# Performance work log

Measured on AMD Instinct MI355X. Metric: run time of the kernel, lower is better.

## Reference

```python
import jax, jax.numpy as jnp
import numpy as np

EPS = 1e-14  # clamp floor from torch .clamp(1e-14)


def setup_inputs() -> dict:
    key = jax.random.key(0)
    kq, kk, kv, km = jax.random.split(key, 4)
    B, L, D = 16, 2048, 64
    q = jax.random.normal(kq, (B, L, D), dtype=jnp.float32)
    k = jax.random.normal(kk, (B, L, D), dtype=jnp.float32)
    v = jax.random.normal(kv, (B, L, D), dtype=jnp.float32)
    # boolean mask, True = masked-out position (score forced to 0 in 'dot' mode)
    attn_mask = jax.random.randint(km, (B, L, L), 0, 2).astype(jnp.bool_)
    return {"q": q, "k": k, "v": v, "attn_mask": attn_mask}


def reference(q, k, v, attn_mask):
    # kernel_type='dot': raw QK^T scores (no temperature scaling)
    attn = jnp.einsum('bqd,bkd->bqk', q, k)
    # masked positions set to 0 (not -inf) in the 'dot' path
    attn = jnp.where(attn_mask, jnp.zeros((), attn.dtype), attn)
    # sum-normalization instead of softmax: attn / attn.sum(-1).clamp(1e-14)
    denom = jnp.clip(jnp.sum(attn, axis=2, keepdims=True), EPS)
    attn = attn / denom
    # dropout is identity at inference (eval mode)
    output = jnp.einsum('bqk,bkd->bqd', attn, v)
    return output, attn
```

## Files before the change

kernel.cpp:

```cpp
#include <hip/hip_runtime.h>

#define Bb 16
#define Lq 2048
#define Dd 64
#define QT 32
#define NT 512

typedef _Float16 f16x2 __attribute__((ext_vector_type(2)));
typedef _Float16 f16x8 __attribute__((ext_vector_type(8)));
typedef __attribute__((ext_vector_type(4))) float f32x4;
typedef __attribute__((ext_vector_type(2))) float f32x2;
typedef __attribute__((ext_vector_type(4))) unsigned int u32x4;
typedef __attribute__((ext_vector_type(2))) unsigned int u32x2;
typedef __attribute__((ext_vector_type(4))) int i32x4;
typedef unsigned long long u64;
typedef __attribute__((ext_vector_type(2))) unsigned long long u64x2;

union H8 { f16x8 v8; f16x2 h2[4]; unsigned int u[4]; u32x4 u4; };
union H1 { f16x2 h; unsigned int u; };

__device__ __forceinline__ f16x2 pkrtz(float a, float b) {
  return __builtin_bit_cast(f16x2, __builtin_amdgcn_cvt_pkrtz(a, b));
}
__device__ __forceinline__ f32x4 MF16(f16x8 a, f16x8 b, f32x4 c) {
  return __builtin_amdgcn_mfma_f32_16x16x32_f16(a, b, c, 0, 0, 0);
}
__device__ __forceinline__ f32x4 MFu(u32x4 a, const H8& b, f32x4 c) {
  return MF16(__builtin_bit_cast(f16x8, a), b.v8, c);
}
__device__ __forceinline__ void gl_lds16(const void* g, void* l) {
  __builtin_amdgcn_global_load_lds(
      (const __attribute__((address_space(1))) void*)g,
      (__attribute__((address_space(3))) void*)l, 16, 0, 0);
}

__global__ __launch_bounds__(256)
void sdpa_prep(const float* __restrict__ kg, const float* __restrict__ vg,
               const i32x4* __restrict__ mg4,
               u32x4* __restrict__ Kw4, u32x4* __restrict__ Vq,
               u64* __restrict__ mb)
{
  const int t = threadIdx.x, blk = blockIdx.x;
  if (blk < 1024) {
    const int row = blk * 32 + (t >> 3);
    const int oct = t & 7;
    const int b = row >> 11, r = row & 2047;
    const int win = r >> 8, rw = r & 255;
    const float* kp = kg + (size_t)row * Dd + oct * 8;
    f32x4 a = *(const f32x4*)kp;
    f32x4 c = *(const f32x4*)(kp + 4);
    H1 h0, h1, h2, h3, l0, l1, l2, l3;
    h0.h = pkrtz(a.x, a.y); l0.h = pkrtz(a.x - (float)h0.h.x, a.y - (float)h0.h.y);
    h1.h = pkrtz(a.z, a.w); l1.h = pkrtz(a.z - (float)h1.h.x, a.w - (float)h1.h.y);
    h2.h = pkrtz(c.x, c.y); l2.h = pkrtz(c.x - (float)h2.h.x, c.y - (float)h2.h.y);
    h3.h = pkrtz(c.z, c.w); l3.h = pkrtz(c.z - (float)h3.h.x, c.w - (float)h3.h.y);
    u32x4 hh = {h0.u, h1.u, h2.u, h3.u};
    u32x4 ll = {l0.u, l1.u, l2.u, l3.u};
    const int sl = oct ^ (rw & 7);
    const size_t base = ((size_t)((b * 8 + win) * 256 + rw)) * 16;
    Kw4[base + sl] = hh;
    Kw4[base + 8 + sl] = ll;
  } else if (blk < 2048) {
    const int v_ = (blk - 1024) * 256 + t;
    const int ln = v_ & 15, nt = (v_ >> 4) & 3, u = (v_ >> 6) & 3;
    const int g = (v_ >> 8) & 7, w = (v_ >> 11) & 7, b = v_ >> 14;
    const int R = w * 256 + g * 32 + u * 4;
    const float* vp = vg + ((size_t)b * Lq + R) * Dd + nt * 16 + ln;
    H1 p0, p1, p2, p3;
    p0.h = pkrtz(vp[0 * Dd],  vp[1 * Dd]);
    p1.h = pkrtz(vp[2 * Dd],  vp[3 * Dd]);
    p2.h = pkrtz(vp[16 * Dd], vp[17 * Dd]);
    p3.h = pkrtz(vp[18 * Dd], vp[19 * Dd]);
    u32x4 o = {p0.u, p1.u, p2.u, p3.u};
    Vq[v_] = o;
  } else {
    const int l  = t & 63;
    const int wg = ((blk - 2048) << 2) | (t >> 6);
    i32x4 cur = __builtin_nontemporal_load(&mg4[((size_t)wg * 32) * 64 + l]);
#pragma unroll 1
    for (int it = 0; it < 32; ++it) {
      i32x4 nxt = {0, 0, 0, 0};
      if (it < 31) nxt = __builtin_nontemporal_load(&mg4[((size_t)wg * 32 + it + 1) * 64 + l]);
      u64 b0 = __ballot(cur.x != 0);
      u64 b1 = __ballot(cur.y != 0);
      u64 b2 = __ballot(cur.z != 0);
      u64 b3 = __ballot(cur.w != 0);
      if (l == 0) {
        u64* o = mb + ((size_t)wg * 32 + it) * 4;
        u64x2 w0 = {b0, b1}, w1 = {b2, b3};
        *(u64x2*)o = w0;
        *(u64x2*)(o + 2) = w1;
      }
      cur = nxt;
    }
  }
}

__global__ __launch_bounds__(NT, 2)
void sdpa_main(const float* __restrict__ qg, const char* __restrict__ Kw,
               const u32x4* __restrict__ Vqp, const u64* __restrict__ mbp,
               float* __restrict__ outO, float* __restrict__ outA)
{
  __shared__ char kbuf[2][65536];
  __shared__ unsigned int Qh[QT][36], Ql[QT][36];
  __shared__ float red[QT][4];
  __shared__ float dinv_s[QT];

  const int tid = threadIdx.x;
  const int l   = tid & 63;
  const int ln  = l & 15;
  const int u   = l >> 4;
  const int w   = tid >> 6;
  const int qt  = w >> 2;
  const int ks  = w & 3;
  const int bid = (int)(blockIdx.x % 8) * 128 + (int)(blockIdx.x / 8);
  const int b   = bid >> 6;
  const int q0  = (bid & 63) * QT;

  {
    int r = tid >> 4, i4 = tid & 15;
    f32x4 qv = *(const f32x4*)(qg + (size_t)(b * Lq + q0 + r) * Dd + 4 * i4);
    H1 ha, hb, la, lb;
    ha.h = pkrtz(qv.x, qv.y); la.h = pkrtz(qv.x - (float)ha.h.x, qv.y - (float)ha.h.y);
    hb.h = pkrtz(qv.z, qv.w); lb.h = pkrtz(qv.z - (float)hb.h.x, qv.w - (float)hb.h.y);
    Qh[r][2 * i4] = ha.u; Qh[r][2 * i4 + 1] = hb.u;
    Ql[r][2 * i4] = la.u; Ql[r][2 * i4 + 1] = lb.u;
  }

  const char* kwb = Kw + (size_t)b * 8 * 65536;
  auto STAGE = [&](int buf_, int win_) {
#pragma unroll
    for (int i = 0; i < 8; ++i)
      gl_lds16(kwb + (size_t)win_ * 65536 + i * 8192 + w * 1024 + l * 16,
               &kbuf[buf_][i * 8192 + w * 1024]);
  };
  STAGE(0, 0);
  __syncthreads();

  H8 Bh0, Bh1, Bl0, Bl1;
  Bh0.u4 = *(const u32x4*)&Qh[16 * qt + ln][4 * u];
  Bh1.u4 = *(const u32x4*)&Qh[16 * qt + ln][16 + 4 * u];
  Bl0.u4 = *(const u32x4*)&Ql[16 * qt + ln][4 * u];
  Bl1.u4 = *(const u32x4*)&Ql[16 * qt + ln][16 + 4 * u];

  const u64* mrow = mbp + (size_t)(b * Lq + q0 + 16 * qt + ln) * 32;
  unsigned int su[8][4][2];
  f32x4 pv[4] = {{0,0,0,0},{0,0,0,0},{0,0,0,0},{0,0,0,0}};
  float rs = 0.f;
  const int key  = ln & 7;
  const int rbase = ks * 64;
  const int shb  = u + ((ks & 1) << 4);
  const bool lowh = (ks < 2);

#pragma unroll
  for (int win = 0; win < 8; ++win) {
    const int cur = win & 1;
    if (win < 7) STAGE(cur ^ 1, win + 1);

    u32x4 vbuf[8];
    const u32x4* vq = Vqp + (size_t)(b * 8 + win) * 2048;
#pragma unroll
    for (int g2 = 0; g2 < 2; ++g2)
#pragma unroll
      for (int nt = 0; nt < 4; ++nt)
        vbuf[g2 * 4 + nt] = vq[(((ks * 2 + g2) * 4 + u) * 4 + nt) * 16 + ln];

    u32x4 MA = *(const u32x4*)(mrow + win * 4);
    u32x4 MC = *(const u32x4*)(mrow + win * 4 + 2);
    unsigned mw0 = lowh ? MA.x : MA.y;
    unsigned mw1 = lowh ? MA.z : MA.w;
    unsigned mw2 = lowh ? MC.x : MC.y;
    unsigned mw3 = lowh ? MC.z : MC.w;

    const char* kb_ = &kbuf[cur][0];
#pragma unroll
    for (int t = 0; t < 4; ++t) {
      const int rw = rbase + 16 * t + ln;
      const char* rp = kb_ + rw * 256;
      u32x4 h0  = *(const u32x4*)(rp + ((u ^ key) << 4));
      u32x4 h1  = *(const u32x4*)(rp + (((4 + u) ^ key) << 4));
      u32x4 l0_ = *(const u32x4*)(rp + ((8 | (u ^ key)) << 4));
      u32x4 l1_ = *(const u32x4*)(rp + ((8 | ((4 + u) ^ key)) << 4));
      f32x4 acc = {0.f, 0.f, 0.f, 0.f};
      acc = MFu(h0, Bh0, acc);
      acc = MFu(h0, Bl0, acc);
      acc = MFu(l0_, Bh0, acc);
      acc = MFu(h1, Bh1, acc);
      acc = MFu(h1, Bl1, acc);
      acc = MFu(l1_, Bh1, acc);
      const int sh = 4 * t + shb;
      float s0 = ((mw0 >> sh) & 1u) ? 0.f : acc.x;
      float s1 = ((mw1 >> sh) & 1u) ? 0.f : acc.y;
      float s2 = ((mw2 >> sh) & 1u) ? 0.f : acc.z;
      float s3 = ((mw3 >> sh) & 1u) ? 0.f : acc.w;
      rs += (s0 + s1) + (s2 + s3);
      H1 p0, p1;
      p0.h = pkrtz(s0, s1); p1.h = pkrtz(s2, s3);
      su[win][t][0] = p0.u; su[win][t][1] = p1.u;
    }
#pragma unroll
    for (int g2 = 0; g2 < 2; ++g2) {
      H8 aw;
      aw.u[0] = su[win][2 * g2][0];     aw.u[1] = su[win][2 * g2][1];
      aw.u[2] = su[win][2 * g2 + 1][0]; aw.u[3] = su[win][2 * g2 + 1][1];
      pv[0] = MF16(aw.v8, __builtin_bit_cast(f16x8, vbuf[g2 * 4 + 0]), pv[0]);
      pv[1] = MF16(aw.v8, __builtin_bit_cast(f16x8, vbuf[g2 * 4 + 1]), pv[1]);
      pv[2] = MF16(aw.v8, __builtin_bit_cast(f16x8, vbuf[g2 * 4 + 2]), pv[2]);
      pv[3] = MF16(aw.v8, __builtin_bit_cast(f16x8, vbuf[g2 * 4 + 3]), pv[3]);
    }
    __syncthreads();
  }

  rs += __shfl_xor(rs, 16);
  rs += __shfl_xor(rs, 32);
  if (l < 16) red[16 * qt + ln][ks] = rs;

  {
    char* Sb = &kbuf[0][0];
    const int row = 16 * qt + ln;
    char* srow = Sb + row * 4096;
    const unsigned skey = (unsigned)(row & 15) << 3;
#pragma unroll
    for (int win = 0; win < 8; ++win)
#pragma unroll
      for (int t = 0; t < 4; ++t) {
        unsigned Bo = 512u * win + 128u * ks + 32u * t + 8u * u;
        u32x2 pk2 = {su[win][t][0], su[win][t][1]};
        *(u32x2*)(srow + (Bo ^ skey)) = pk2;
      }
  }
  __syncthreads();
  if (tid < 32) {
    f32x4 r4 = *(const f32x4*)&red[tid][0];
    float s = (r4.x + r4.y) + (r4.z + r4.w);
    dinv_s[tid] = 1.0f / fmaxf(s, 1e-14f);
  }
  __syncthreads();

  {
    const char* Sb = &kbuf[0][0];
#pragma unroll
    for (int r = 0; r < 4; ++r) {
      const int rr = 4 * w + r;
      const float dv = dinv_s[rr];
      const char* sr = Sb + rr * 4096;
      const unsigned rk = (unsigned)(rr & 15) << 3;
      float* arow = outA + (size_t)(b * Lq + q0 + rr) * Lq;
#pragma unroll
      for (int m = 0; m < 8; ++m) {
        u32x2 pk = *(const u32x2*)(sr + ((unsigned)(512 * m + 8 * l) ^ rk));
        H1 a0, a1; a0.u = pk.x; a1.u = pk.y;
        f32x4 st = {(float)a0.h.x * dv, (float)a0.h.y * dv,
                    (float)a1.h.x * dv, (float)a1.h.y * dv};
        __builtin_nontemporal_store(st, (f32x4*)(arow + 256 * m + 4 * l));
      }
    }
  }
  __syncthreads();

  {
    float (*Or)[4][16][66] = (float (*)[4][16][66])&kbuf[0][0];
#pragma unroll
    for (int nt = 0; nt < 4; ++nt)
#pragma unroll
      for (int r2 = 0; r2 < 4; ++r2)
        Or[qt][ks][4 * u + r2][16 * nt + ln] = pv[nt][r2];
    __syncthreads();
#pragma unroll
    for (int i = 0; i < 2; ++i) {
      int item = tid + NT * i;
      int q_ = item >> 5, d = (item & 31) * 2;
      float o0 = 0.f, o1 = 0.f;
#pragma unroll
      for (int k2 = 0; k2 < 4; ++k2) {
        o0 += Or[q_ >> 4][k2][q_ & 15][d];
        o1 += Or[q_ >> 4][k2][q_ & 15][d + 1];
      }
      float dv = dinv_s[q_];
      f32x2 st = {o0 * dv, o1 * dv};
      *(f32x2*)(outO + (size_t)(b * Lq + q0 + q_) * Dd + d) = st;
    }
  }
}

extern "C" void kernel_launch(void* const* d_in, const int* in_sizes, int n_in,
                              void* d_out, int out_size, void* d_ws, size_t ws_size,
                              hipStream_t stream) {
  const float* q = (const float*)d_in[0];
  const float* k = (const float*)d_in[1];
  const float* v = (const float*)d_in[2];
  const int*   m = (const int*)d_in[3];
  float* outO = (float*)d_out;
  float* outA = outO + (size_t)Bb * Lq * Dd;

  char* ws = (char*)d_ws;
  u32x4* Kw4 = (u32x4*)ws;
  u32x4* Vq  = (u32x4*)(ws + (8u << 20));
  u64*   mb  = (u64*)(ws + (12u << 20));
  sdpa_prep<<<4096, 256, 0, stream>>>(k, v, (const i32x4*)m, Kw4, Vq, mb);
  sdpa_main<<<Bb * (Lq / QT), NT, 0, stream>>>(q, (const char*)Kw4, Vq, mb, outO, outA);
}
```

Before: 162.4 us.

## Defer PV MFMA to post-normalization pass and write attn directly from registers

Moves the P·V MFMA accumulation out of the QK score loop into a second loop that runs after the row sums are known. That second loop double-buffers V register loads one window ahead. The attention matrix is now written straight from the register-held fp16 scores, scaled by the inverse denominator, so the LDS staging round trip and its extra barriers go away. The cost is that each lane's stores now cover only 16-byte chunks within 64-float segments instead of fully contiguous 256-float row sweeps, which may hurt store coalescing. Register pressure also rises from the doubled V buffer.

```diff
diff --git a/kernel.cpp b/kernel.cpp
--- a/kernel.cpp
+++ b/kernel.cpp
@@ -145,25 +145,16 @@
 
   const u64* mrow = mbp + (size_t)(b * Lq + q0 + 16 * qt + ln) * 32;
   unsigned int su[8][4][2];
-  f32x4 pv[4] = {{0,0,0,0},{0,0,0,0},{0,0,0,0},{0,0,0,0}};
   float rs = 0.f;
-  const int key  = ln & 7;
+  const int key   = ln & 7;
   const int rbase = ks * 64;
-  const int shb  = u + ((ks & 1) << 4);
+  const int shb   = u + ((ks & 1) << 4);
   const bool lowh = (ks < 2);
 
 #pragma unroll
   for (int win = 0; win < 8; ++win) {
     const int cur = win & 1;
     if (win < 7) STAGE(cur ^ 1, win + 1);
-
-    u32x4 vbuf[8];
-    const u32x4* vq = Vqp + (size_t)(b * 8 + win) * 2048;
-#pragma unroll
-    for (int g2 = 0; g2 < 2; ++g2)
-#pragma unroll
-      for (int nt = 0; nt < 4; ++nt)
-        vbuf[g2 * 4 + nt] = vq[(((ks * 2 + g2) * 4 + u) * 4 + nt) * 16 + ln];
 
     u32x4 MA = *(const u32x4*)(mrow + win * 4);
     u32x4 MC = *(const u32x4*)(mrow + win * 4 + 2);
@@ -198,37 +189,12 @@
       p0.h = pkrtz(s0, s1); p1.h = pkrtz(s2, s3);
       su[win][t][0] = p0.u; su[win][t][1] = p1.u;
     }
-#pragma unroll
-    for (int g2 = 0; g2 < 2; ++g2) {
-      H8 aw;
-      aw.u[0] = su[win][2 * g2][0];     aw.u[1] = su[win][2 * g2][1];
-      aw.u[2] = su[win][2 * g2 + 1][0]; aw.u[3] = su[win][2 * g2 + 1][1];
-      pv[0] = MF16(aw.v8, __builtin_bit_cast(f16x8, vbuf[g2 * 4 + 0]), pv[0]);
-      pv[1] = MF16(aw.v8, __builtin_bit_cast(f16x8, vbuf[g2 * 4 + 1]), pv[1]);
-      pv[2] = MF16(aw.v8, __builtin_bit_cast(f16x8, vbuf[g2 * 4 + 2]), pv[2]);
-      pv[3] = MF16(aw.v8, __builtin_bit_cast(f16x8, vbuf[g2 * 4 + 3]), pv[3]);
-    }
     __syncthreads();
   }
 
   rs += __shfl_xor(rs, 16);
   rs += __shfl_xor(rs, 32);
   if (l < 16) red[16 * qt + ln][ks] = rs;
-
-  {
-    char* Sb = &kbuf[0][0];
-    const int row = 16 * qt + ln;
-    char* srow = Sb + row * 4096;
-    const unsigned skey = (unsigned)(row & 15) << 3;
-#pragma unroll
-    for (int win = 0; win < 8; ++win)
-#pragma unroll
-      for (int t = 0; t < 4; ++t) {
-        unsigned Bo = 512u * win + 128u * ks + 32u * t + 8u * u;
-        u32x2 pk2 = {su[win][t][0], su[win][t][1]};
-        *(u32x2*)(srow + (Bo ^ skey)) = pk2;
-      }
-  }
   __syncthreads();
   if (tid < 32) {
     f32x4 r4 = *(const f32x4*)&red[tid][0];
@@ -237,26 +203,47 @@
   }
   __syncthreads();
 
-  {
-    const char* Sb = &kbuf[0][0];
-#pragma unroll
-    for (int r = 0; r < 4; ++r) {
-      const int rr = 4 * w + r;
-      const float dv = dinv_s[rr];
-      const char* sr = Sb + rr * 4096;
-      const unsigned rk = (unsigned)(rr & 15) << 3;
-      float* arow = outA + (size_t)(b * Lq + q0 + rr) * Lq;
-#pragma unroll
-      for (int m = 0; m < 8; ++m) {
-        u32x2 pk = *(const u32x2*)(sr + ((unsigned)(512 * m + 8 * l) ^ rk));
-        H1 a0, a1; a0.u = pk.x; a1.u = pk.y;
-        f32x4 st = {(float)a0.h.x * dv, (float)a0.h.y * dv,
-                    (float)a1.h.x * dv, (float)a1.h.y * dv};
-        __builtin_nontemporal_store(st, (f32x4*)(arow + 256 * m + 4 * l));
-      }
-    }
-  }
-  __syncthreads();
+  f32x4 pv[4] = {{0,0,0,0},{0,0,0,0},{0,0,0,0},{0,0,0,0}};
+  const float dv = dinv_s[16 * qt + ln];
+  float* arow = outA + (size_t)(b * Lq + q0 + 16 * qt + ln) * Lq + ks * 64;
+
+  u32x4 vb[2][8];
+#pragma unroll
+  for (int g2 = 0; g2 < 2; ++g2)
+#pragma unroll
+    for (int nt = 0; nt < 4; ++nt)
+      vb[0][g2 * 4 + nt] =
+          Vqp[(size_t)(b * 8) * 2048 + (((ks * 2 + g2) * 4 + u) * 4 + nt) * 16 + ln];
+
+#pragma unroll
+  for (int win = 0; win < 8; ++win) {
+    const int c2 = win & 1;
+    if (win < 7) {
+      const u32x4* vqn = Vqp + (size_t)(b * 8 + win + 1) * 2048;
+#pragma unroll
+      for (int g2 = 0; g2 < 2; ++g2)
+#pragma unroll
+        for (int nt = 0; nt < 4; ++nt)
+          vb[c2 ^ 1][g2 * 4 + nt] = vqn[(((ks * 2 + g2) * 4 + u) * 4 + nt) * 16 + ln];
+    }
+#pragma unroll
+    for (int t = 0; t < 4; ++t) {
+      H1 p0, p1; p0.u = su[win][t][0]; p1.u = su[win][t][1];
+      f32x4 st = {(float)p0.h.x * dv, (float)p0.h.y * dv,
+                  (float)p1.h.x * dv, (float)p1.h.y * dv};
+      __builtin_nontemporal_store(st, (f32x4*)(arow + win * 256 + 16 * t + 4 * u));
+    }
+#pragma unroll
+    for (int g2 = 0; g2 < 2; ++g2) {
+      H8 aw;
+      aw.u[0] = su[win][2 * g2][0];     aw.u[1] = su[win][2 * g2][1];
+      aw.u[2] = su[win][2 * g2 + 1][0]; aw.u[3] = su[win][2 * g2 + 1][1];
+      pv[0] = MF16(aw.v8, __builtin_bit_cast(f16x8, vb[c2][g2 * 4 + 0]), pv[0]);
+      pv[1] = MF16(aw.v8, __builtin_bit_cast(f16x8, vb[c2][g2 * 4 + 1]), pv[1]);
+      pv[2] = MF16(aw.v8, __builtin_bit_cast(f16x8, vb[c2][g2 * 4 + 2]), pv[2]);
+      pv[3] = MF16(aw.v8, __builtin_bit_cast(f16x8, vb[c2][g2 * 4 + 3]), pv[3]);
+    }
+  }
 
   {
     float (*Or)[4][16][66] = (float (*)[4][16][66])&kbuf[0][0];
@@ -276,8 +263,8 @@
         o0 += Or[q_ >> 4][k2][q_ & 15][d];
         o1 += Or[q_ >> 4][k2][q_ & 15][d + 1];
       }
-      float dv = dinv_s[q_];
-      f32x2 st = {o0 * dv, o1 * dv};
+      float dvq = dinv_s[q_];
+      f32x2 st = {o0 * dvq, o1 * dvq};
       *(f32x2*)(outO + (size_t)(b * Lq + q0 + q_) * Dd + d) = st;
     }
   }
```

Measured after the change: 186.5 us. +14.9%, slower.

## Halve K window size to shrink LDS footprint and raise occupancy

Applied to the files above, without the earlier changes.

Splits the key dimension into 16 windows of 128 rows instead of 8 of 256, halving the double-buffered K LDS tile. The goal is to fit more workgroups per CU (launch bounds raised from 2 to 4 blocks). The attention-row writeback is restaged in two halves so the score buffer fits in the smaller LDS. The trade-offs are twice as many barriers and window iterations, a tighter register budget per thread, and extra syncs in the output phase.

```diff
diff --git a/kernel.cpp b/kernel.cpp
--- a/kernel.cpp
+++ b/kernel.cpp
@@ -5,6 +5,8 @@
 #define Dd 64
 #define QT 32
 #define NT 512
+#define NWIN 16
+#define WINB 32768
 
 typedef _Float16 f16x2 __attribute__((ext_vector_type(2)));
 typedef _Float16 f16x8 __attribute__((ext_vector_type(8)));
@@ -45,7 +47,7 @@
     const int row = blk * 32 + (t >> 3);
     const int oct = t & 7;
     const int b = row >> 11, r = row & 2047;
-    const int win = r >> 8, rw = r & 255;
+    const int win = r >> 7, rw = r & 127;
     const float* kp = kg + (size_t)row * Dd + oct * 8;
     f32x4 a = *(const f32x4*)kp;
     f32x4 c = *(const f32x4*)(kp + 4);
@@ -57,7 +59,7 @@
     u32x4 hh = {h0.u, h1.u, h2.u, h3.u};
     u32x4 ll = {l0.u, l1.u, l2.u, l3.u};
     const int sl = oct ^ (rw & 7);
-    const size_t base = ((size_t)((b * 8 + win) * 256 + rw)) * 16;
+    const size_t base = ((size_t)((b * 16 + win) * 128 + rw)) * 16;
     Kw4[base + sl] = hh;
     Kw4[base + 8 + sl] = ll;
   } else if (blk < 2048) {
@@ -96,12 +98,12 @@
   }
 }
 
-__global__ __launch_bounds__(NT, 2)
+__global__ __launch_bounds__(NT, 4)
 void sdpa_main(const float* __restrict__ qg, const char* __restrict__ Kw,
                const u32x4* __restrict__ Vqp, const u64* __restrict__ mbp,
                float* __restrict__ outO, float* __restrict__ outA)
 {
-  __shared__ char kbuf[2][65536];
+  __shared__ char kbuf[2][WINB];
   __shared__ unsigned int Qh[QT][36], Ql[QT][36];
   __shared__ float red[QT][4];
   __shared__ float dinv_s[QT];
@@ -127,11 +129,11 @@
     Ql[r][2 * i4] = la.u; Ql[r][2 * i4 + 1] = lb.u;
   }
 
-  const char* kwb = Kw + (size_t)b * 8 * 65536;
+  const char* kwb = Kw + (size_t)b * NWIN * WINB;
   auto STAGE = [&](int buf_, int win_) {
 #pragma unroll
-    for (int i = 0; i < 8; ++i)
-      gl_lds16(kwb + (size_t)win_ * 65536 + i * 8192 + w * 1024 + l * 16,
+    for (int i = 0; i < 4; ++i)
+      gl_lds16(kwb + (size_t)win_ * WINB + i * 8192 + w * 1024 + l * 16,
                &kbuf[buf_][i * 8192 + w * 1024]);
   };
   STAGE(0, 0);
@@ -144,37 +146,39 @@
   Bl1.u4 = *(const u32x4*)&Ql[16 * qt + ln][16 + 4 * u];
 
   const u64* mrow = mbp + (size_t)(b * Lq + q0 + 16 * qt + ln) * 32;
-  unsigned int su[8][4][2];
+  unsigned int su[NWIN][2][2];
   f32x4 pv[4] = {{0,0,0,0},{0,0,0,0},{0,0,0,0},{0,0,0,0}};
   float rs = 0.f;
-  const int key  = ln & 7;
-  const int rbase = ks * 64;
-  const int shb  = u + ((ks & 1) << 4);
-  const bool lowh = (ks < 2);
-
-#pragma unroll
-  for (int win = 0; win < 8; ++win) {
+  const int key   = ln & 7;
+  const int rbase = ks * 32;
+  u32x4 MA, MC;
+
+#pragma unroll
+  for (int win = 0; win < NWIN; ++win) {
     const int cur = win & 1;
-    if (win < 7) STAGE(cur ^ 1, win + 1);
-
-    u32x4 vbuf[8];
-    const u32x4* vq = Vqp + (size_t)(b * 8 + win) * 2048;
-#pragma unroll
-    for (int g2 = 0; g2 < 2; ++g2)
+    if (win < NWIN - 1) STAGE(cur ^ 1, win + 1);
+
+    if ((win & 1) == 0) {
+      MA = *(const u32x4*)(mrow + (win >> 1) * 4);
+      MC = *(const u32x4*)(mrow + (win >> 1) * 4 + 2);
+    }
+    unsigned mw0 = (win & 1) ? MA.y : MA.x;
+    unsigned mw1 = (win & 1) ? MA.w : MA.z;
+    unsigned mw2 = (win & 1) ? MC.y : MC.x;
+    unsigned mw3 = (win & 1) ? MC.w : MC.z;
+
+    u32x4 vbuf[4];
+    {
+      const u32x4* vq = Vqp + (size_t)(b * 8 + (win >> 1)) * 2048;
+      const int g_old = (win & 1) * 4 + ks;
 #pragma unroll
       for (int nt = 0; nt < 4; ++nt)
-        vbuf[g2 * 4 + nt] = vq[(((ks * 2 + g2) * 4 + u) * 4 + nt) * 16 + ln];
-
-    u32x4 MA = *(const u32x4*)(mrow + win * 4);
-    u32x4 MC = *(const u32x4*)(mrow + win * 4 + 2);
-    unsigned mw0 = lowh ? MA.x : MA.y;
-    unsigned mw1 = lowh ? MA.z : MA.w;
-    unsigned mw2 = lowh ? MC.x : MC.y;
-    unsigned mw3 = lowh ? MC.z : MC.w;
+        vbuf[nt] = vq[((g_old * 4 + u) * 4 + nt) * 16 + ln];
+    }
 
     const char* kb_ = &kbuf[cur][0];
 #pragma unroll
-    for (int t = 0; t < 4; ++t) {
+    for (int t = 0; t < 2; ++t) {
       const int rw = rbase + 16 * t + ln;
       const char* rp = kb_ + rw * 256;
       u32x4 h0  = *(const u32x4*)(rp + ((u ^ key) << 4));
@@ -188,7 +192,7 @@
       acc = MFu(h1, Bh1, acc);
       acc = MFu(h1, Bl1, acc);
       acc = MFu(l1_, Bh1, acc);
-      const int sh = 4 * t + shb;
+      const int sh = ks * 8 + 4 * t + u;
       float s0 = ((mw0 >> sh) & 1u) ? 0.f : acc.x;
       float s1 = ((mw1 >> sh) & 1u) ? 0.f : acc.y;
       float s2 = ((mw2 >> sh) & 1u) ? 0.f : acc.z;
@@ -198,15 +202,14 @@
       p0.h = pkrtz(s0, s1); p1.h = pkrtz(s2, s3);
       su[win][t][0] = p0.u; su[win][t][1] = p1.u;
     }
-#pragma unroll
-    for (int g2 = 0; g2 < 2; ++g2) {
+    {
       H8 aw;
-      aw.u[0] = su[win][2 * g2][0];     aw.u[1] = su[win][2 * g2][1];
-      aw.u[2] = su[win][2 * g2 + 1][0]; aw.u[3] = su[win][2 * g2 + 1][1];
-      pv[0] = MF16(aw.v8, __builtin_bit_cast(f16x8, vbuf[g2 * 4 + 0]), pv[0]);
-      pv[1] = MF16(aw.v8, __builtin_bit_cast(f16x8, vbuf[g2 * 4 + 1]), pv[1]);
-      pv[2] = MF16(aw.v8, __builtin_bit_cast(f16x8, vbuf[g2 * 4 + 2]), pv[2]);
-      pv[3] = MF16(aw.v8, __builtin_bit_cast(f16x8, vbuf[g2 * 4 + 3]), pv[3]);
+      aw.u[0] = su[win][0][0]; aw.u[1] = su[win][0][1];
+      aw.u[2] = su[win][1][0]; aw.u[3] = su[win][1][1];
+      pv[0] = MF16(aw.v8, __builtin_bit_cast(f16x8, vbuf[0]), pv[0]);
+      pv[1] = MF16(aw.v8, __builtin_bit_cast(f16x8, vbuf[1]), pv[1]);
+      pv[2] = MF16(aw.v8, __builtin_bit_cast(f16x8, vbuf[2]), pv[2]);
+      pv[3] = MF16(aw.v8, __builtin_bit_cast(f16x8, vbuf[3]), pv[3]);
     }
     __syncthreads();
   }
@@ -214,21 +217,6 @@
   rs += __shfl_xor(rs, 16);
   rs += __shfl_xor(rs, 32);
   if (l < 16) red[16 * qt + ln][ks] = rs;
-
-  {
-    char* Sb = &kbuf[0][0];
-    const int row = 16 * qt + ln;
-    char* srow = Sb + row * 4096;
-    const unsigned skey = (unsigned)(row & 15) << 3;
-#pragma unroll
-    for (int win = 0; win < 8; ++win)
-#pragma unroll
-      for (int t = 0; t < 4; ++t) {
-        unsigned Bo = 512u * win + 128u * ks + 32u * t + 8u * u;
-        u32x2 pk2 = {su[win][t][0], su[win][t][1]};
-        *(u32x2*)(srow + (Bo ^ skey)) = pk2;
-      }
-  }
   __syncthreads();
   if (tid < 32) {
     f32x4 r4 = *(const f32x4*)&red[tid][0];
@@ -237,14 +225,29 @@
   }
   __syncthreads();
 
-  {
-    const char* Sb = &kbuf[0][0];
-#pragma unroll
-    for (int r = 0; r < 4; ++r) {
-      const int rr = 4 * w + r;
+  char* Sb = &kbuf[0][0];
+#pragma unroll
+  for (int half = 0; half < 2; ++half) {
+    if (qt == half) {
+      char* srow = Sb + ln * 4096;
+      const unsigned skey = (unsigned)ln << 3;
+#pragma unroll
+      for (int win = 0; win < NWIN; ++win)
+#pragma unroll
+        for (int t = 0; t < 2; ++t) {
+          unsigned Bo = 256u * win + 64u * ks + 32u * t + 8u * u;
+          u32x2 pk2 = {su[win][t][0], su[win][t][1]};
+          *(u32x2*)(srow + (Bo ^ skey)) = pk2;
+        }
+    }
+    __syncthreads();
+#pragma unroll
+    for (int r = 0; r < 2; ++r) {
+      const int rl = 2 * w + r;
+      const int rr = 16 * half + rl;
       const float dv = dinv_s[rr];
-      const char* sr = Sb + rr * 4096;
-      const unsigned rk = (unsigned)(rr & 15) << 3;
+      const char* sr = Sb + rl * 4096;
+      const unsigned rk = (unsigned)rl << 3;
       float* arow = outA + (size_t)(b * Lq + q0 + rr) * Lq;
 #pragma unroll
       for (int m = 0; m < 8; ++m) {
@@ -255,8 +258,8 @@
         __builtin_nontemporal_store(st, (f32x4*)(arow + 256 * m + 4 * l));
       }
     }
-  }
-  __syncthreads();
+    __syncthreads();
+  }
 
   {
     float (*Or)[4][16][66] = (float (*)[4][16][66])&kbuf[0][0];
@@ -276,8 +279,8 @@
         o0 += Or[q_ >> 4][k2][q_ & 15][d];
         o1 += Or[q_ >> 4][k2][q_ & 15][d + 1];
       }
-      float dv = dinv_s[q_];
-      f32x2 st = {o0 * dv, o1 * dv};
+      float dvq = dinv_s[q_];
+      f32x2 st = {o0 * dvq, o1 * dvq};
       *(f32x2*)(outO + (size_t)(b * Lq + q0 + q_) * Dd + d) = st;
     }
   }
```

After: 169.7 us. +4.5%, slower.
